# Optimization experiments

Measured on AMD Instinct MI355X. Metric: run time of the kernel, lower is better.

The kernel has to match this reference:

```python
import jax, jax.numpy as jnp
import numpy as np

N_NODES = 250000


def _glorot(key, shape):
    fan_in, fan_out = shape[0], shape[1]
    lim = jnp.sqrt(6.0 / (fan_in + fan_out))
    return jax.random.uniform(key, shape, jnp.float32, -lim, lim)


def setup_inputs() -> dict:
    key = jax.random.key(0)
    ks = jax.random.split(key, 16)
    x = jax.random.normal(ks[0], (N_NODES, 9), jnp.float32)
    edge_index = jax.random.randint(ks[1], (2, 5000000), 0, N_NODES, jnp.int64)
    return {
        "x": x,
        "edge_index": edge_index,
        "W1": _glorot(ks[2], (9, 16)),  "b1": jnp.zeros((16,), jnp.float32),
        "W2": _glorot(ks[3], (16, 16)), "b2": jnp.zeros((16,), jnp.float32),
        "W3": _glorot(ks[4], (16, 16)), "b3": jnp.zeros((16,), jnp.float32),
        "Wl2": _glorot(ks[5], (25, 128)),  "bl2": jnp.zeros((128,), jnp.float32),
        "Wl3": _glorot(ks[6], (128, 128)), "bl3": jnp.zeros((128,), jnp.float32),
        "Wl4": _glorot(ks[7], (128, 1)),   "bl4": jnp.zeros((1,), jnp.float32),
    }


def _gcn_conv(x, src, dst, norm, W, b, n):
    # PyG GCNConv: linear transform, then D^-1/2 (A+I) D^-1/2 aggregation, then bias
    h = x @ W                                   # [N, d_out]
    msg = h[src] * norm[:, None]                # gather + scale   [E+N, d_out]
    agg = jax.ops.segment_sum(msg, dst, num_segments=n)
    return agg + b


def _sym_norm(src, dst, n):
    deg = jax.ops.segment_sum(jnp.ones_like(dst, jnp.float32), dst, num_segments=n)
    dinv = jnp.where(deg > 0, jax.lax.rsqrt(deg), 0.0)
    return dinv[src] * dinv[dst]


def reference(x, edge_index, W1, b1, W2, b2, W3, b3, Wl2, bl2, Wl3, bl3, Wl4, bl4):
    n = x.shape[0]
    loops = jnp.arange(n, dtype=edge_index.dtype)
    src = jnp.concatenate([edge_index[0], loops])  # add self loops
    dst = jnp.concatenate([edge_index[1], loops])
    norm = _sym_norm(src, dst, n)  # same graph for all 3 conv layers

    h = jax.nn.relu(_gcn_conv(x, src, dst, norm, W1, b1, n))
    h = jax.nn.relu(_gcn_conv(h, src, dst, norm, W2, b2, n))
    h = jax.nn.relu(_gcn_conv(h, src, dst, norm, W3, b3, n))

    h = jnp.concatenate([x, h], axis=1)          # [N, 25]
    h = jax.nn.relu(h @ Wl2 + bl2)
    h = jax.nn.relu(h @ Wl3 + bl3)
    return h @ Wl4 + bl4                         # [N, 1]
```

## Files before the change

kernel.cpp:

```cpp
#include <hip/hip_runtime.h>


#define NBLK 512
#define BSH  9
#define BSZ  512
#define MAXNB 1024

__global__ __launch_bounds__(64) void k_detect(const void* __restrict__ edges,
                                               int* __restrict__ flag, int n_nodes)
{
    if (threadIdx.x == 0 && blockIdx.x == 0) {
        const long long* p = (const long long*)edges;
        int is64 = 1;
        for (int i = 0; i < 16; ++i) {
            long long v = p[i];
            if (v < 0 || v >= (long long)n_nodes) is64 = 0;
        }
        *flag = is64;
    }
}

__device__ __forceinline__ int ld_idx(const void* edges, int f64, long long idx)
{
    return f64 ? ((const int*)edges)[idx << 1] : ((const int*)edges)[idx];
}

__global__ __launch_bounds__(256) void k_hist2(const void* __restrict__ edges,
                                               const int* __restrict__ flag,
                                               int* __restrict__ cnt_blk,
                                               long long E, int NB)
{
    __shared__ int cnt[MAXNB];
    int tid = threadIdx.x;
    for (int b = tid; b < NB; b += 256) cnt[b] = 0;
    __syncthreads();
    int f64 = *flag;
    long long chunk = (E + NBLK - 1) / NBLK;
    long long lo = (long long)blockIdx.x * chunk;
    long long hi = lo + chunk; if (hi > E) hi = E;
    for (long long i = lo + tid; i < hi; i += 256) {
        int d = ld_idx(edges, f64, E + i);
        atomicAdd(&cnt[d >> BSH], 1);
    }
    __syncthreads();
    for (int b = tid; b < NB; b += 256)
        cnt_blk[(size_t)b * NBLK + blockIdx.x] = (cnt[b] + 15) & ~15;
}

__global__ __launch_bounds__(256) void k_scan1(const int* __restrict__ in,
                                               int* __restrict__ excl,
                                               int* __restrict__ partials, int n)
{
    __shared__ int s[256];
    int tid = threadIdx.x;
    int i = blockIdx.x * 256 + tid;
    int v = (i < n) ? in[i] : 0;
    s[tid] = v;
    __syncthreads();
#pragma unroll
    for (int off = 1; off < 256; off <<= 1) {
        int t = (tid >= off) ? s[tid - off] : 0;
        __syncthreads();
        s[tid] += t;
        __syncthreads();
    }
    if (i < n) excl[i] = s[tid] - v;
    if (tid == 255) partials[blockIdx.x] = s[255];
}

__global__ __launch_bounds__(1024) void k_scan2(int* __restrict__ p, int nb)
{
    __shared__ int s[1024];
    __shared__ int carry_s;
    int t = threadIdx.x;
    if (t == 0) carry_s = 0;
    __syncthreads();
    for (int base = 0; base < nb; base += 1024) {
        int idx = base + t;
        int v = (idx < nb) ? p[idx] : 0;
        s[t] = v;
        __syncthreads();
        for (int off = 1; off < 1024; off <<= 1) {
            int u = (t >= off) ? s[t - off] : 0;
            __syncthreads();
            s[t] += u;
            __syncthreads();
        }
        int carry = carry_s;
        if (idx < nb) p[idx] = carry + s[t] - v;
        __syncthreads();
        if (t == 0) carry_s += s[1023];
        __syncthreads();
    }
}

__global__ __launch_bounds__(256) void k_scan3(int* __restrict__ excl,
                                               const int* __restrict__ partials, int n)
{
    int i = blockIdx.x * 256 + threadIdx.x;
    if (i < n) excl[i] += partials[blockIdx.x];
}

__global__ __launch_bounds__(256) void k_bin(const void* __restrict__ edges,
                                             const int* __restrict__ flag,
                                             const int* __restrict__ base_blk,
                                             int* __restrict__ epk,
                                             long long E, int NB)
{
    __shared__ int cnt[MAXNB];
    __shared__ int base[MAXNB];
    __shared__ int cur[MAXNB];
    int tid = threadIdx.x;
    for (int b = tid; b < NB; b += 256) cnt[b] = 0;
    __syncthreads();
    int f64 = *flag;
    long long chunk = (E + NBLK - 1) / NBLK;
    long long lo = (long long)blockIdx.x * chunk;
    long long hi = lo + chunk; if (hi > E) hi = E;
    for (long long i = lo + tid; i < hi; i += 256) {
        int d = ld_idx(edges, f64, E + i);
        atomicAdd(&cnt[d >> BSH], 1);
    }
    __syncthreads();
    for (int b = tid; b < NB; b += 256) {
        base[b] = base_blk[(size_t)b * NBLK + blockIdx.x];
        cur[b] = 0;
    }
    __syncthreads();
    for (long long i = lo + tid; i < hi; i += 256) {
        int s = ld_idx(edges, f64, i);
        int d = ld_idx(edges, f64, E + i);
        int b = d >> BSH;
        int slot = atomicAdd(&cur[b], 1);
        epk[base[b] + slot] = ((d & (BSZ - 1)) << 18) | s;
    }
    __syncthreads();
    for (int b = tid; b < NB; b += 256) {
        int c = cnt[b];
        int r = (c + 15) & ~15;
        for (int j = c; j < r; ++j) epk[base[b] + j] = -1;
    }
}

__global__ __launch_bounds__(256) void k_csr(const int* __restrict__ epk,
                                             const int* __restrict__ base_blk,
                                             int* __restrict__ csr,
                                             int* __restrict__ row_off,
                                             int* __restrict__ degi,
                                             float* __restrict__ dinv, int n)
{
    __shared__ int cnt[BSZ];
    __shared__ int off[BSZ];
    __shared__ int ps[256];
    int b = blockIdx.x;
    int tid = threadIdx.x;
    int start = base_blk[(size_t)b * NBLK];
    int end   = base_blk[(size_t)(b + 1) * NBLK];
    cnt[tid] = 0; cnt[tid + 256] = 0;
    __syncthreads();
    for (int e = start + tid; e < end; e += 256) {
        int pk = epk[e];
        if (pk >= 0) atomicAdd(&cnt[pk >> 18], 1);
    }
    __syncthreads();
    int pairSum = cnt[2 * tid] + cnt[2 * tid + 1];
    ps[tid] = pairSum;
    __syncthreads();
#pragma unroll
    for (int o = 1; o < 256; o <<= 1) {
        int v = (tid >= o) ? ps[tid - o] : 0;
        __syncthreads();
        ps[tid] += v;
        __syncthreads();
    }
    int incl = ps[tid];
    off[2 * tid]     = incl - pairSum;
    off[2 * tid + 1] = incl - pairSum + cnt[2 * tid];
    __syncthreads();
    int nbase = b << BSH;
#pragma unroll
    for (int l = tid; l < BSZ; l += 256) {
        int node = nbase + l;
        if (node < n) {
            row_off[node] = start + off[l];
            degi[node]    = cnt[l];
            dinv[node]    = rsqrtf((float)cnt[l] + 1.0f);
        }
    }
    __syncthreads();
    for (int e = start + tid; e < end; e += 256) {
        int pk = epk[e];
        if (pk < 0) continue;
        int l = pk >> 18;
        int pos = atomicAdd(&off[l], 1);
        csr[start + pos] = pk & 0x3FFFF;
    }
}

__global__ __launch_bounds__(256) void k_lin1(const float* __restrict__ x,
                                              const float* __restrict__ W1,
                                              const float* __restrict__ dinv,
                                              float* __restrict__ hs, int n)
{
    __shared__ float sW[144];
    if (threadIdx.x < 144) sW[threadIdx.x] = W1[threadIdx.x];
    __syncthreads();
    int i = blockIdx.x * 256 + threadIdx.x;
    if (i >= n) return;
    float xv[9];
#pragma unroll
    for (int k = 0; k < 9; ++k) xv[k] = x[(size_t)i * 9 + k];
    float di = dinv[i];
#pragma unroll
    for (int j = 0; j < 16; ++j) {
        float acc = 0.f;
#pragma unroll
        for (int k = 0; k < 9; ++k) acc = fmaf(xv[k], sW[k * 16 + j], acc);
        hs[(size_t)i * 16 + j] = acc * di;
    }
}

template<int MODE>
__global__ __launch_bounds__(256) void k_gatherF(const int* __restrict__ csr,
                                                 const int* __restrict__ row_off,
                                                 const int* __restrict__ degi,
                                                 const float* __restrict__ dinv,
                                                 const float* __restrict__ hs,
                                                 const float* __restrict__ W,
                                                 const float* __restrict__ bias,
                                                 float* __restrict__ outb, int n)
{
    int wid = (int)(((long long)blockIdx.x * 256 + threadIdx.x) >> 6);
    if (wid >= n) return;
    int lane = threadIdx.x & 63;
    int slot = lane >> 2;
    int q    = lane & 3;
    int start = row_off[wid];
    int deg   = degi[wid];
    float di  = dinv[wid];
    float4 sum;
    if (slot == 0) sum = *(const float4*)&hs[(size_t)wid * 16 + q * 4];
    else           sum = make_float4(0.f, 0.f, 0.f, 0.f);
    int e = slot;
    for (; e + 16 < deg; e += 32) {
        int s0 = csr[start + e];
        int s1 = csr[start + e + 16];
        float4 v0 = *(const float4*)&hs[(size_t)s0 * 16 + q * 4];
        float4 v1 = *(const float4*)&hs[(size_t)s1 * 16 + q * 4];
        sum.x += v0.x + v1.x; sum.y += v0.y + v1.y;
        sum.z += v0.z + v1.z; sum.w += v0.w + v1.w;
    }
    if (e < deg) {
        int s0 = csr[start + e];
        float4 v0 = *(const float4*)&hs[(size_t)s0 * 16 + q * 4];
        sum.x += v0.x; sum.y += v0.y; sum.z += v0.z; sum.w += v0.w;
    }
#pragma unroll
    for (int off = 4; off < 64; off <<= 1) {
        sum.x += __shfl_xor(sum.x, off);
        sum.y += __shfl_xor(sum.y, off);
        sum.z += __shfl_xor(sum.z, off);
        sum.w += __shfl_xor(sum.w, off);
    }
    float4 aq = make_float4(sum.x * di, sum.y * di, sum.z * di, sum.w * di);

    if (MODE == 0) {
        if (slot == 0) *(float4*)&outb[(size_t)wid * 16 + q * 4] = aq;
    } else {
        float t[16];
#pragma unroll
        for (int a = 0; a < 4; ++a) {
            t[4 * a + 0] = __shfl(aq.x, a);
            t[4 * a + 1] = __shfl(aq.y, a);
            t[4 * a + 2] = __shfl(aq.z, a);
            t[4 * a + 3] = __shfl(aq.w, a);
        }
#pragma unroll
        for (int k = 0; k < 16; ++k) {
            float v = t[k] + bias[k];
            t[k] = v > 0.f ? v : 0.f;
        }
        int j = lane & 15;
        float o = 0.f;
#pragma unroll
        for (int k = 0; k < 16; ++k)
            o = fmaf(t[k], W[k * 16 + j], o);
        if (lane < 16) outb[(size_t)wid * 16 + j] = o * di;
    }
}

__global__ __launch_bounds__(256) void k_mlp(const float* __restrict__ x,
                                             const float* __restrict__ agg3,
                                             const float* __restrict__ b3,
                                             const float* __restrict__ Wl2,
                                             const float* __restrict__ bl2,
                                             const float* __restrict__ Wl3,
                                             const float* __restrict__ bl3,
                                             const float* __restrict__ Wl4,
                                             const float* __restrict__ bl4,
                                             float* __restrict__ out, int n)
{
    __shared__ __align__(16) float zs[4][16][128];

    int tid  = threadIdx.x;
    int w    = tid >> 6;
    int lane = tid & 63;
    int og   = lane & 15;
    int ng   = lane >> 4;
    int base = (blockIdx.x * 4 + w) * 16;

    for (int idx = lane; idx < 16 * 25; idx += 64) {
        int nn = idx / 25, f = idx - nn * 25;
        int node = base + nn;
        float v = 0.f;
        if (node < n) {
            if (f < 9) v = x[(size_t)node * 9 + f];
            else {
                float t = agg3[(size_t)node * 16 + (f - 9)] + b3[f - 9];
                v = t > 0.f ? t : 0.f;
            }
        }
        zs[w][nn][f] = v;
    }
    __syncthreads();

    float acc[4][8];
    {
        float4 b0 = *(const float4*)&bl2[og * 8];
        float4 b1 = *(const float4*)&bl2[og * 8 + 4];
#pragma unroll
        for (int i = 0; i < 4; ++i) {
            acc[i][0] = b0.x; acc[i][1] = b0.y; acc[i][2] = b0.z; acc[i][3] = b0.w;
            acc[i][4] = b1.x; acc[i][5] = b1.y; acc[i][6] = b1.z; acc[i][7] = b1.w;
        }
    }
#pragma unroll
    for (int k = 0; k < 25; ++k) {
        float4 w0 = *(const float4*)&Wl2[k * 128 + og * 8];
        float4 w1 = *(const float4*)&Wl2[k * 128 + og * 8 + 4];
#pragma unroll
        for (int i = 0; i < 4; ++i) {
            float f = zs[w][ng * 4 + i][k];
            acc[i][0] = fmaf(f, w0.x, acc[i][0]); acc[i][1] = fmaf(f, w0.y, acc[i][1]);
            acc[i][2] = fmaf(f, w0.z, acc[i][2]); acc[i][3] = fmaf(f, w0.w, acc[i][3]);
            acc[i][4] = fmaf(f, w1.x, acc[i][4]); acc[i][5] = fmaf(f, w1.y, acc[i][5]);
            acc[i][6] = fmaf(f, w1.z, acc[i][6]); acc[i][7] = fmaf(f, w1.w, acc[i][7]);
        }
    }
    __syncthreads();
    {
        int c0 = (og * 8) ^ (ng << 3);
#pragma unroll
        for (int i = 0; i < 4; ++i) {
            float4 lo, hi;
            lo.x = acc[i][0] > 0.f ? acc[i][0] : 0.f; lo.y = acc[i][1] > 0.f ? acc[i][1] : 0.f;
            lo.z = acc[i][2] > 0.f ? acc[i][2] : 0.f; lo.w = acc[i][3] > 0.f ? acc[i][3] : 0.f;
            hi.x = acc[i][4] > 0.f ? acc[i][4] : 0.f; hi.y = acc[i][5] > 0.f ? acc[i][5] : 0.f;
            hi.z = acc[i][6] > 0.f ? acc[i][6] : 0.f; hi.w = acc[i][7] > 0.f ? acc[i][7] : 0.f;
            *(float4*)&zs[w][ng * 4 + i][c0]     = lo;
            *(float4*)&zs[w][ng * 4 + i][c0 + 4] = hi;
        }
    }
    __syncthreads();

    {
        float4 b0 = *(const float4*)&bl3[og * 8];
        float4 b1 = *(const float4*)&bl3[og * 8 + 4];
#pragma unroll
        for (int i = 0; i < 4; ++i) {
            acc[i][0] = b0.x; acc[i][1] = b0.y; acc[i][2] = b0.z; acc[i][3] = b0.w;
            acc[i][4] = b1.x; acc[i][5] = b1.y; acc[i][6] = b1.z; acc[i][7] = b1.w;
        }
    }
    int swz = ng << 3;
#pragma unroll 2
    for (int k4 = 0; k4 < 64; k4 += 4) {
        float4 z4[4];
#pragma unroll
        for (int i = 0; i < 4; ++i)
            z4[i] = *(const float4*)&zs[w][ng * 4 + i][k4 ^ swz];
#pragma unroll
        for (int kk = 0; kk < 4; ++kk) {
            const float* wr = &Wl3[(k4 + kk) * 128 + og * 8];
            float4 w0 = *(const float4*)wr;
            float4 w1 = *(const float4*)(wr + 4);
#pragma unroll
            for (int i = 0; i < 4; ++i) {
                float zz = (kk == 0) ? z4[i].x : (kk == 1) ? z4[i].y
                         : (kk == 2) ? z4[i].z : z4[i].w;
                acc[i][0] = fmaf(zz, w0.x, acc[i][0]); acc[i][1] = fmaf(zz, w0.y, acc[i][1]);
                acc[i][2] = fmaf(zz, w0.z, acc[i][2]); acc[i][3] = fmaf(zz, w0.w, acc[i][3]);
                acc[i][4] = fmaf(zz, w1.x, acc[i][4]); acc[i][5] = fmaf(zz, w1.y, acc[i][5]);
                acc[i][6] = fmaf(zz, w1.z, acc[i][6]); acc[i][7] = fmaf(zz, w1.w, acc[i][7]);
            }
        }
    }
    __syncthreads();
#pragma unroll 2
    for (int k4 = 64; k4 < 128; k4 += 4) {
        float4 z4[4];
#pragma unroll
        for (int i = 0; i < 4; ++i)
            z4[i] = *(const float4*)&zs[w][ng * 4 + i][k4 ^ swz];
#pragma unroll
        for (int kk = 0; kk < 4; ++kk) {
            const float* wr = &Wl3[(k4 + kk) * 128 + og * 8];
            float4 w0 = *(const float4*)wr;
            float4 w1 = *(const float4*)(wr + 4);
#pragma unroll
            for (int i = 0; i < 4; ++i) {
                float zz = (kk == 0) ? z4[i].x : (kk == 1) ? z4[i].y
                         : (kk == 2) ? z4[i].z : z4[i].w;
                acc[i][0] = fmaf(zz, w0.x, acc[i][0]); acc[i][1] = fmaf(zz, w0.y, acc[i][1]);
                acc[i][2] = fmaf(zz, w0.z, acc[i][2]); acc[i][3] = fmaf(zz, w0.w, acc[i][3]);
                acc[i][4] = fmaf(zz, w1.x, acc[i][4]); acc[i][5] = fmaf(zz, w1.y, acc[i][5]);
                acc[i][6] = fmaf(zz, w1.z, acc[i][6]); acc[i][7] = fmaf(zz, w1.w, acc[i][7]);
            }
        }
    }

    {
        float4 w40 = *(const float4*)&Wl4[og * 8];
        float4 w41 = *(const float4*)&Wl4[og * 8 + 4];
        float bb = bl4[0];
#pragma unroll
        for (int i = 0; i < 4; ++i) {
            float p = 0.f;
            p = fmaf(acc[i][0] > 0.f ? acc[i][0] : 0.f, w40.x, p);
            p = fmaf(acc[i][1] > 0.f ? acc[i][1] : 0.f, w40.y, p);
            p = fmaf(acc[i][2] > 0.f ? acc[i][2] : 0.f, w40.z, p);
            p = fmaf(acc[i][3] > 0.f ? acc[i][3] : 0.f, w40.w, p);
            p = fmaf(acc[i][4] > 0.f ? acc[i][4] : 0.f, w41.x, p);
            p = fmaf(acc[i][5] > 0.f ? acc[i][5] : 0.f, w41.y, p);
            p = fmaf(acc[i][6] > 0.f ? acc[i][6] : 0.f, w41.z, p);
            p = fmaf(acc[i][7] > 0.f ? acc[i][7] : 0.f, w41.w, p);
            p += __shfl_xor(p, 1);
            p += __shfl_xor(p, 2);
            p += __shfl_xor(p, 4);
            p += __shfl_xor(p, 8);
            int node = base + ng * 4 + i;
            if (og == 0 && node < n) out[node] = p + bb;
        }
    }
}

extern "C" void kernel_launch(void* const* d_in, const int* in_sizes, int n_in,
                              void* d_out, int out_size, void* d_ws, size_t ws_size,
                              hipStream_t stream)
{
    const float* x   = (const float*)d_in[0];
    const void*  ei  = d_in[1];
    const float* W1  = (const float*)d_in[2];
    const float* b1  = (const float*)d_in[3];
    const float* W2  = (const float*)d_in[4];
    const float* b2  = (const float*)d_in[5];
    const float* W3  = (const float*)d_in[6];
    const float* b3  = (const float*)d_in[7];
    const float* Wl2 = (const float*)d_in[8];
    const float* bl2 = (const float*)d_in[9];
    const float* Wl3 = (const float*)d_in[10];
    const float* bl3 = (const float*)d_in[11];
    const float* Wl4 = (const float*)d_in[12];
    const float* bl4 = (const float*)d_in[13];
    float* out = (float*)d_out;

    int n        = in_sizes[0] / 9;
    long long e2 = (long long)in_sizes[1];
    long long E  = e2 / 2;
    int NB       = (n + BSZ - 1) >> BSH;
    int L        = NB * NBLK + 1;
    size_t EPAD  = (size_t)E + (size_t)NBLK * NB * 16;

    char* ws = (char*)d_ws;
    size_t off = 0;
    int*   flag     = (int*)(ws + off); off += 256;
    int*   cnt_blk  = (int*)(ws + off); off += (size_t)L * 4;        off = (off + 255) & ~(size_t)255;
    int*   base_blk = (int*)(ws + off); off += (size_t)L * 4;        off = (off + 255) & ~(size_t)255;
    int*   partials = (int*)(ws + off); off += 16384;
    float* dinv     = (float*)(ws + off); off += (size_t)n * 4;      off = (off + 255) & ~(size_t)255;
    int*   degi     = (int*)(ws + off); off += (size_t)n * 4;        off = (off + 255) & ~(size_t)255;
    int*   row_off  = (int*)(ws + off); off += (size_t)n * 4;        off = (off + 255) & ~(size_t)255;
    int*   csr      = (int*)(ws + off); off += EPAD * 4;             off = (off + 255) & ~(size_t)255;
    int*   epk      = (int*)(ws + off); off += EPAD * 4;             off = (off + 255) & ~(size_t)255;
    float* bufA = (float*)epk;
    float* bufB = bufA + (size_t)n * 16;

    int nb_n = (n + 255) / 256;
    int nb_s = (L + 255) / 256;

    k_detect<<<1, 64, 0, stream>>>(ei, flag, n);
    hipMemsetAsync(cnt_blk + (L - 1), 0, 4, stream);
    k_hist2<<<NBLK, 256, 0, stream>>>(ei, flag, cnt_blk, E, NB);
    k_scan1<<<nb_s, 256, 0, stream>>>(cnt_blk, base_blk, partials, L);
    k_scan2<<<1, 1024, 0, stream>>>(partials, nb_s);
    k_scan3<<<nb_s, 256, 0, stream>>>(base_blk, partials, L);
    k_bin<<<NBLK, 256, 0, stream>>>(ei, flag, base_blk, epk, E, NB);
    k_csr<<<NB, 256, 0, stream>>>(epk, base_blk, csr, row_off, degi, dinv, n);

    int nb_g = (n + 3) / 4;
    k_lin1<<<nb_n, 256, 0, stream>>>(x, W1, dinv, bufA, n);
    k_gatherF<1><<<nb_g, 256, 0, stream>>>(csr, row_off, degi, dinv, bufA, W2, b1,
                                           bufB, n);
    k_gatherF<1><<<nb_g, 256, 0, stream>>>(csr, row_off, degi, dinv, bufB, W3, b2,
                                           bufA, n);
    k_gatherF<0><<<nb_g, 256, 0, stream>>>(csr, row_off, degi, dinv, bufA, nullptr,
                                           nullptr, bufB, n);
    k_mlp<<<(n + 63) / 64, 256, 0, stream>>>(x, bufB, b3, Wl2, bl2, Wl3, bl3, Wl4, bl4,
                                             out, n);
}
```

Before: 593.3 us.

## Run MLP head on bf16 MFMA with pre-transposed bf16 weights

```diff
diff --git a/kernel.cpp b/kernel.cpp
--- a/kernel.cpp
+++ b/kernel.cpp
@@ -5,6 +5,16 @@
 #define BSH  9
 #define BSZ  512
 #define MAXNB 1024
+
+typedef __attribute__((ext_vector_type(8))) __bf16 bf16x8;
+typedef __attribute__((ext_vector_type(4))) float  f32x4;
+
+__device__ __forceinline__ unsigned short f2b(float f)
+{
+    unsigned u = __float_as_uint(f);
+    unsigned r = (u + 0x7FFFu + ((u >> 16) & 1u)) >> 16;
+    return (unsigned short)r;
+}
 
 __global__ __launch_bounds__(64) void k_detect(const void* __restrict__ edges,
                                                int* __restrict__ flag, int n_nodes)
@@ -289,158 +299,118 @@
     }
 }
 
+__global__ __launch_bounds__(256) void k_cvt(const float* __restrict__ Wl2,
+                                             const float* __restrict__ Wl3,
+                                             unsigned short* __restrict__ Wl2T,
+                                             unsigned short* __restrict__ Wl3T)
+{
+    int i = blockIdx.x * 256 + threadIdx.x;
+    if (i < 128 * 32) {
+        int c = i >> 5, k = i & 31;
+        float v = (k < 25) ? Wl2[k * 128 + c] : 0.f;
+        Wl2T[i] = f2b(v);
+    }
+    int j = i - 128 * 32;
+    if (j >= 0 && j < 128 * 128) {
+        int c = j >> 7, k = j & 127;
+        Wl3T[j] = f2b(Wl3[k * 128 + c]);
+    }
+}
+
 __global__ __launch_bounds__(256) void k_mlp(const float* __restrict__ x,
                                              const float* __restrict__ agg3,
                                              const float* __restrict__ b3,
-                                             const float* __restrict__ Wl2,
+                                             const unsigned short* __restrict__ Wl2T,
                                              const float* __restrict__ bl2,
-                                             const float* __restrict__ Wl3,
+                                             const unsigned short* __restrict__ Wl3T,
                                              const float* __restrict__ bl3,
                                              const float* __restrict__ Wl4,
                                              const float* __restrict__ bl4,
                                              float* __restrict__ out, int n)
 {
-    __shared__ __align__(16) float zs[4][16][128];
+    __shared__ __align__(16) unsigned short featb[4][16 * 40];
+    __shared__ __align__(16) unsigned short zb[4][16 * 128];
 
     int tid  = threadIdx.x;
     int w    = tid >> 6;
     int lane = tid & 63;
-    int og   = lane & 15;
-    int ng   = lane >> 4;
+    int g    = lane >> 4;
+    int l15  = lane & 15;
     int base = (blockIdx.x * 4 + w) * 16;
 
-    for (int idx = lane; idx < 16 * 25; idx += 64) {
-        int nn = idx / 25, f = idx - nn * 25;
+    for (int idx = lane; idx < 16 * 32; idx += 64) {
+        int nn = idx >> 5, f = idx & 31;
         int node = base + nn;
         float v = 0.f;
         if (node < n) {
             if (f < 9) v = x[(size_t)node * 9 + f];
-            else {
+            else if (f < 25) {
                 float t = agg3[(size_t)node * 16 + (f - 9)] + b3[f - 9];
                 v = t > 0.f ? t : 0.f;
             }
         }
-        zs[w][nn][f] = v;
-    }
-    __syncthreads();
-
-    float acc[4][8];
-    {
-        float4 b0 = *(const float4*)&bl2[og * 8];
-        float4 b1 = *(const float4*)&bl2[og * 8 + 4];
-#pragma unroll
-        for (int i = 0; i < 4; ++i) {
-            acc[i][0] = b0.x; acc[i][1] = b0.y; acc[i][2] = b0.z; acc[i][3] = b0.w;
-            acc[i][4] = b1.x; acc[i][5] = b1.y; acc[i][6] = b1.z; acc[i][7] = b1.w;
-        }
-    }
-#pragma unroll
-    for (int k = 0; k < 25; ++k) {
-        float4 w0 = *(const float4*)&Wl2[k * 128 + og * 8];
-        float4 w1 = *(const float4*)&Wl2[k * 128 + og * 8 + 4];
-#pragma unroll
-        for (int i = 0; i < 4; ++i) {
-            float f = zs[w][ng * 4 + i][k];
-            acc[i][0] = fmaf(f, w0.x, acc[i][0]); acc[i][1] = fmaf(f, w0.y, acc[i][1]);
-            acc[i][2] = fmaf(f, w0.z, acc[i][2]); acc[i][3] = fmaf(f, w0.w, acc[i][3]);
-            acc[i][4] = fmaf(f, w1.x, acc[i][4]); acc[i][5] = fmaf(f, w1.y, acc[i][5]);
-            acc[i][6] = fmaf(f, w1.z, acc[i][6]); acc[i][7] = fmaf(f, w1.w, acc[i][7]);
-        }
-    }
-    __syncthreads();
-    {
-        int c0 = (og * 8) ^ (ng << 3);
-#pragma unroll
-        for (int i = 0; i < 4; ++i) {
-            float4 lo, hi;
-            lo.x = acc[i][0] > 0.f ? acc[i][0] : 0.f; lo.y = acc[i][1] > 0.f ? acc[i][1] : 0.f;
-            lo.z = acc[i][2] > 0.f ? acc[i][2] : 0.f; lo.w = acc[i][3] > 0.f ? acc[i][3] : 0.f;
-            hi.x = acc[i][4] > 0.f ? acc[i][4] : 0.f; hi.y = acc[i][5] > 0.f ? acc[i][5] : 0.f;
-            hi.z = acc[i][6] > 0.f ? acc[i][6] : 0.f; hi.w = acc[i][7] > 0.f ? acc[i][7] : 0.f;
-            *(float4*)&zs[w][ng * 4 + i][c0]     = lo;
-            *(float4*)&zs[w][ng * 4 + i][c0 + 4] = hi;
-        }
-    }
-    __syncthreads();
-
-    {
-        float4 b0 = *(const float4*)&bl3[og * 8];
-        float4 b1 = *(const float4*)&bl3[og * 8 + 4];
-#pragma unroll
-        for (int i = 0; i < 4; ++i) {
-            acc[i][0] = b0.x; acc[i][1] = b0.y; acc[i][2] = b0.z; acc[i][3] = b0.w;
-            acc[i][4] = b1.x; acc[i][5] = b1.y; acc[i][6] = b1.z; acc[i][7] = b1.w;
-        }
-    }
-    int swz = ng << 3;
-#pragma unroll 2
-    for (int k4 = 0; k4 < 64; k4 += 4) {
-        float4 z4[4];
-#pragma unroll
-        for (int i = 0; i < 4; ++i)
-            z4[i] = *(const float4*)&zs[w][ng * 4 + i][k4 ^ swz];
-#pragma unroll
-        for (int kk = 0; kk < 4; ++kk) {
-            const float* wr = &Wl3[(k4 + kk) * 128 + og * 8];
-            float4 w0 = *(const float4*)wr;
-            float4 w1 = *(const float4*)(wr + 4);
-#pragma unroll
-            for (int i = 0; i < 4; ++i) {
-                float zz = (kk == 0) ? z4[i].x : (kk == 1) ? z4[i].y
-                         : (kk == 2) ? z4[i].z : z4[i].w;
-                acc[i][0] = fmaf(zz, w0.x, acc[i][0]); acc[i][1] = fmaf(zz, w0.y, acc[i][1]);
-                acc[i][2] = fmaf(zz, w0.z, acc[i][2]); acc[i][3] = fmaf(zz, w0.w, acc[i][3]);
-                acc[i][4] = fmaf(zz, w1.x, acc[i][4]); acc[i][5] = fmaf(zz, w1.y, acc[i][5]);
-                acc[i][6] = fmaf(zz, w1.z, acc[i][6]); acc[i][7] = fmaf(zz, w1.w, acc[i][7]);
-            }
-        }
-    }
-    __syncthreads();
-#pragma unroll 2
-    for (int k4 = 64; k4 < 128; k4 += 4) {
-        float4 z4[4];
-#pragma unroll
-        for (int i = 0; i < 4; ++i)
-            z4[i] = *(const float4*)&zs[w][ng * 4 + i][k4 ^ swz];
-#pragma unroll
-        for (int kk = 0; kk < 4; ++kk) {
-            const float* wr = &Wl3[(k4 + kk) * 128 + og * 8];
-            float4 w0 = *(const float4*)wr;
-            float4 w1 = *(const float4*)(wr + 4);
-#pragma unroll
-            for (int i = 0; i < 4; ++i) {
-                float zz = (kk == 0) ? z4[i].x : (kk == 1) ? z4[i].y
-                         : (kk == 2) ? z4[i].z : z4[i].w;
-                acc[i][0] = fmaf(zz, w0.x, acc[i][0]); acc[i][1] = fmaf(zz, w0.y, acc[i][1]);
-                acc[i][2] = fmaf(zz, w0.z, acc[i][2]); acc[i][3] = fmaf(zz, w0.w, acc[i][3]);
-                acc[i][4] = fmaf(zz, w1.x, acc[i][4]); acc[i][5] = fmaf(zz, w1.y, acc[i][5]);
-                acc[i][6] = fmaf(zz, w1.z, acc[i][6]); acc[i][7] = fmaf(zz, w1.w, acc[i][7]);
-            }
-        }
-    }
-
-    {
-        float4 w40 = *(const float4*)&Wl4[og * 8];
-        float4 w41 = *(const float4*)&Wl4[og * 8 + 4];
-        float bb = bl4[0];
-#pragma unroll
-        for (int i = 0; i < 4; ++i) {
-            float p = 0.f;
-            p = fmaf(acc[i][0] > 0.f ? acc[i][0] : 0.f, w40.x, p);
-            p = fmaf(acc[i][1] > 0.f ? acc[i][1] : 0.f, w40.y, p);
-            p = fmaf(acc[i][2] > 0.f ? acc[i][2] : 0.f, w40.z, p);
-            p = fmaf(acc[i][3] > 0.f ? acc[i][3] : 0.f, w40.w, p);
-            p = fmaf(acc[i][4] > 0.f ? acc[i][4] : 0.f, w41.x, p);
-            p = fmaf(acc[i][5] > 0.f ? acc[i][5] : 0.f, w41.y, p);
-            p = fmaf(acc[i][6] > 0.f ? acc[i][6] : 0.f, w41.z, p);
-            p = fmaf(acc[i][7] > 0.f ? acc[i][7] : 0.f, w41.w, p);
-            p += __shfl_xor(p, 1);
-            p += __shfl_xor(p, 2);
-            p += __shfl_xor(p, 4);
-            p += __shfl_xor(p, 8);
-            int node = base + ng * 4 + i;
-            if (og == 0 && node < n) out[node] = p + bb;
-        }
+        featb[w][nn * 40 + f] = f2b(v);
+    }
+    __syncthreads();
+
+    bf16x8 a2 = *(const bf16x8*)&featb[w][l15 * 40 + 8 * g];
+    char* zbw = (char*)&zb[w][0];
+#pragma unroll
+    for (int t = 0; t < 8; ++t) {
+        int col = l15 + 16 * t;
+        bf16x8 b2 = *(const bf16x8*)&Wl2T[(size_t)col * 32 + 8 * g];
+        f32x4 c = {0.f, 0.f, 0.f, 0.f};
+        c = __builtin_amdgcn_mfma_f32_16x16x32_bf16(a2, b2, c, 0, 0, 0);
+        float bb = bl2[col];
+#pragma unroll
+        for (int r = 0; r < 4; ++r) {
+            int node = g * 4 + r;
+            float v = c[r] + bb;
+            v = v > 0.f ? v : 0.f;
+            int byte = node * 256 + ((2 * col) ^ ((node & 7) << 4));
+            *(unsigned short*)(zbw + byte) = f2b(v);
+        }
+    }
+    __syncthreads();
+
+    f32x4 acc[8];
+#pragma unroll
+    for (int t = 0; t < 8; ++t) acc[t] = (f32x4){0.f, 0.f, 0.f, 0.f};
+#pragma unroll
+    for (int s = 0; s < 4; ++s) {
+        int kb = 8 * g + 32 * s;
+        int byteA = l15 * 256 + ((2 * kb) ^ ((l15 & 7) << 4));
+        bf16x8 a3 = *(const bf16x8*)(zbw + byteA);
+#pragma unroll
+        for (int t = 0; t < 8; ++t) {
+            bf16x8 b3f = *(const bf16x8*)&Wl3T[(size_t)(l15 + 16 * t) * 128 + kb];
+            acc[t] = __builtin_amdgcn_mfma_f32_16x16x32_bf16(a3, b3f, acc[t], 0, 0, 0);
+        }
+    }
+
+    float p[4] = {0.f, 0.f, 0.f, 0.f};
+#pragma unroll
+    for (int t = 0; t < 8; ++t) {
+        int col = l15 + 16 * t;
+        float b3v = bl3[col];
+        float w4  = Wl4[col];
+#pragma unroll
+        for (int r = 0; r < 4; ++r) {
+            float v = acc[t][r] + b3v;
+            v = v > 0.f ? v : 0.f;
+            p[r] = fmaf(v, w4, p[r]);
+        }
+    }
+    float bb = bl4[0];
+#pragma unroll
+    for (int r = 0; r < 4; ++r) {
+        float s = p[r];
+        s += __shfl_xor(s, 1);
+        s += __shfl_xor(s, 2);
+        s += __shfl_xor(s, 4);
+        s += __shfl_xor(s, 8);
+        int node = base + g * 4 + r;
+        if (l15 == 0 && node < n) out[node] = s + bb;
     }
 }
 
@@ -477,6 +447,10 @@
     int*   cnt_blk  = (int*)(ws + off); off += (size_t)L * 4;        off = (off + 255) & ~(size_t)255;
     int*   base_blk = (int*)(ws + off); off += (size_t)L * 4;        off = (off + 255) & ~(size_t)255;
     int*   partials = (int*)(ws + off); off += 16384;
+    unsigned short* wl2t = (unsigned short*)(ws + off); off += 128 * 32 * 2;
+    off = (off + 255) & ~(size_t)255;
+    unsigned short* wl3t = (unsigned short*)(ws + off); off += 128 * 128 * 2;
+    off = (off + 255) & ~(size_t)255;
     float* dinv     = (float*)(ws + off); off += (size_t)n * 4;      off = (off + 255) & ~(size_t)255;
     int*   degi     = (int*)(ws + off); off += (size_t)n * 4;        off = (off + 255) & ~(size_t)255;
     int*   row_off  = (int*)(ws + off); off += (size_t)n * 4;        off = (off + 255) & ~(size_t)255;
@@ -490,6 +464,7 @@
 
     k_detect<<<1, 64, 0, stream>>>(ei, flag, n);
     hipMemsetAsync(cnt_blk + (L - 1), 0, 4, stream);
+    k_cvt<<<80, 256, 0, stream>>>(Wl2, Wl3, wl2t, wl3t);
     k_hist2<<<NBLK, 256, 0, stream>>>(ei, flag, cnt_blk, E, NB);
     k_scan1<<<nb_s, 256, 0, stream>>>(cnt_blk, base_blk, partials, L);
     k_scan2<<<1, 1024, 0, stream>>>(partials, nb_s);
@@ -505,6 +480,6 @@
                                            bufA, n);
     k_gatherF<0><<<nb_g, 256, 0, stream>>>(csr, row_off, degi, dinv, bufA, nullptr,
                                            nullptr, bufB, n);
-    k_mlp<<<(n + 63) / 64, 256, 0, stream>>>(x, bufB, b3, Wl2, bl2, Wl3, bl3, Wl4, bl4,
-                                             out, n);
-}
+    k_mlp<<<(n + 63) / 64, 256, 0, stream>>>(x, bufB, b3, wl2t, bl2, wl3t, bl3,
+                                             Wl4, bl4, out, n);
+}
```

Result: faster. 522.3 us (-12.0%).
